# Performance work log

Measured on AMD Instinct MI355X. Metric: run time of the kernel, lower is better.

## Reference

```python
import jax, jax.numpy as jnp
import numpy as np

BLOCK_SIZE = 16
NVFP4_LEVELS = np.array([0.0, 0.5, 1.0, 1.5, 2.0, 3.0, 4.0, 6.0], dtype=np.float32)


def quantize_to_nvfp4(x, block_size=BLOCK_SIZE):
    """NVFP4 fake-quant: per-16-element block, scale = amax/6, round |x| to nearest level."""
    levels = jnp.asarray(NVFP4_LEVELS, dtype=x.dtype)
    orig_shape = x.shape
    xf = x.reshape(-1, block_size)                                   # [nblk, 16]
    amax = jnp.clip(jnp.max(jnp.abs(xf), axis=-1, keepdims=True), 1e-12)
    scale = amax / 6.0                                               # [nblk, 1]
    x_norm = jnp.abs(xf) / scale                                     # in [0, 6]
    idx = jnp.argmin(jnp.abs(x_norm[..., None] - levels), axis=-1)   # nearest level (first on ties, like torch)
    x_q = jnp.sign(xf) * levels[idx] * scale
    return x_q.reshape(orig_shape)


def _magnitude_mask_2_4(w):
    # keep 2 largest-|.| of every group of 4 along in_features (row-wise 2:4)
    out_f, in_f = w.shape
    a = jnp.abs(w).reshape(out_f, in_f // 4, 4)
    thr = jnp.sort(a, axis=-1)[..., 2:3]          # 2nd-largest magnitude in group
    mask = (a >= thr).reshape(out_f, in_f)
    return mask.astype(w.dtype)


def setup_inputs() -> dict:
    key = jax.random.key(0)
    k_x, k_w, k_s, k_a, k_b, k_bias = jax.random.split(key, 6)
    B, S, IN_F, OUT_F, RANK = 2, 2048, 4096, 4096, 32
    x = jax.random.normal(k_x, (B, S, IN_F), dtype=jnp.float32)
    smooth_scale = jax.random.uniform(k_s, (IN_F,), dtype=jnp.float32, minval=0.5, maxval=2.0)
    # realistic calibrated weight: 2:4 magnitude-sparse then NVFP4 fake-quantized
    w = jax.random.normal(k_w, (OUT_F, IN_F), dtype=jnp.float32) * 0.02
    w_sparse = w * _magnitude_mask_2_4(w)
    w_quantized = quantize_to_nvfp4(w_sparse)
    lora_a = jax.random.normal(k_a, (RANK, IN_F), dtype=jnp.float32) * 0.02
    lora_b = jax.random.normal(k_b, (OUT_F, RANK), dtype=jnp.float32) * 0.02
    bias = jax.random.normal(k_bias, (OUT_F,), dtype=jnp.float32)
    return {"x": x, "smooth_scale": smooth_scale, "w_quantized": w_quantized,
            "lora_a": lora_a, "lora_b": lora_b, "bias": bias}


def reference(x, smooth_scale, w_quantized, lora_a, lora_b, bias):
    # x: [B, S, IN], smooth_scale: [IN], w_quantized: [OUT, IN]
    x_smoothed = x * smooth_scale                                    # SmoothQuant activation scaling
    x_q = quantize_to_nvfp4(x_smoothed, BLOCK_SIZE)                  # block fake-quant of activations
    base_out = jnp.einsum('bsi,oi->bso', x_q, w_quantized)           # 2:4-sparse quantized matmul
    svd_out = jnp.einsum('bsr,or->bso',
                         jnp.einsum('bsi,ri->bsr', x_smoothed, lora_a), lora_b)  # low-rank correction
    return base_out + svd_out + bias
```

## Files before the change

### kernel.cpp

```cpp
#include <hip/hip_runtime.h>
#include <hip/hip_bf16.h>
#include <stdint.h>

typedef __attribute__((ext_vector_type(8)))  __bf16 bf16x8;
typedef __attribute__((ext_vector_type(4)))  float  f32x4;

#define KP 4224

__device__ inline void async_copy16(const void* g, void* l) {
  __builtin_amdgcn_global_load_lds((const __attribute__((address_space(1))) void*)g,
                                   (__attribute__((address_space(3))) void*)l, 16, 0, 0);
}

__global__ __launch_bounds__(256) void fused_quant_lora_kernel(
    const float* __restrict__ x, const float* __restrict__ ss,
    const float* __restrict__ la, __bf16* __restrict__ Ab,
    float* __restrict__ Tp) {
  __shared__ float red[4][16][32];
  int tid  = threadIdx.x;
  int m0   = blockIdx.x << 4;
  int by   = blockIdx.y;

  {
    int row = m0 + (tid >> 4);
    int cb0 = tid & 15;
#pragma unroll
    for (int i = 0; i < 2; i++) {
      int col = (by << 9) + ((cb0 + (i << 4)) << 4);
      const float4* xp = (const float4*)(x + ((size_t)row << 12) + col);
      const float4* sp = (const float4*)(ss + col);
      float xs[16];
#pragma unroll
      for (int j = 0; j < 4; j++) {
        float4 xv = xp[j]; float4 sv = sp[j];
        xs[4*j+0] = xv.x * sv.x; xs[4*j+1] = xv.y * sv.y;
        xs[4*j+2] = xv.z * sv.z; xs[4*j+3] = xv.w * sv.w;
      }
      float amax = 0.f;
#pragma unroll
      for (int j = 0; j < 16; j++) amax = fmaxf(amax, fabsf(xs[j]));
      amax = fmaxf(amax, 1e-12f);
      float scale = amax / 6.0f;
      bf16x8 o0, o1;
#pragma unroll
      for (int j = 0; j < 16; j++) {
        float a  = fabsf(xs[j]);
        float xn = a / scale;
        float lvl;
        if (xn < 2.25f) {
          lvl = 0.5f * __builtin_ceilf(__builtin_fmaf(2.0f, xn, -0.5f));
        } else {
          lvl = (xn <= 2.5f) ? 2.0f : (xn <= 3.5f) ? 3.0f
              : (xn <= 5.0f) ? 4.0f : 6.0f;
        }
        float mag = lvl * scale;
        float q = (xs[j] > 0.f) ? mag : ((xs[j] < 0.f) ? -mag : 0.f);
        if (j < 8) o0[j] = (__bf16)q; else o1[j-8] = (__bf16)q;
      }
      __bf16* dst = Ab + (size_t)row * KP + col;
      *(bf16x8*)dst = o0;
      *(bf16x8*)(dst + 8) = o1;
    }
  }

  {
    int wave = tid >> 6, lane = tid & 63;
    int lrow = lane & 15, kg = lane >> 4;
    int kbase = (by << 9) + (wave << 7);
    f32x4 acc0 = {0.f,0.f,0.f,0.f}, acc1 = {0.f,0.f,0.f,0.f};
    const float* xrow = x + ((size_t)(m0 + lrow) << 12);
    const float* a0   = la + ((size_t)lrow << 12);
    const float* a1   = a0 + (16 << 12);
#pragma unroll
    for (int k0 = 0; k0 < 128; k0 += 32) {
      int kk = kbase + k0 + (kg << 3);
      float xv[8], sv[8], v0[8], v1[8];
      *(float4*)&xv[0] = *(const float4*)(xrow + kk);
      *(float4*)&xv[4] = *(const float4*)(xrow + kk + 4);
      *(float4*)&sv[0] = *(const float4*)(ss + kk);
      *(float4*)&sv[4] = *(const float4*)(ss + kk + 4);
      *(float4*)&v0[0] = *(const float4*)(a0 + kk);
      *(float4*)&v0[4] = *(const float4*)(a0 + kk + 4);
      *(float4*)&v1[0] = *(const float4*)(a1 + kk);
      *(float4*)&v1[4] = *(const float4*)(a1 + kk + 4);
      bf16x8 af, b0, b1;
#pragma unroll
      for (int j = 0; j < 8; j++) {
        af[j] = (__bf16)(xv[j] * sv[j]);
        b0[j] = (__bf16)v0[j];
        b1[j] = (__bf16)v1[j];
      }
      acc0 = __builtin_amdgcn_mfma_f32_16x16x32_bf16(af, b0, acc0, 0, 0, 0);
      acc1 = __builtin_amdgcn_mfma_f32_16x16x32_bf16(af, b1, acc1, 0, 0, 0);
    }
#pragma unroll
    for (int r = 0; r < 4; r++) {
      red[wave][kg*4 + r][lrow]      = acc0[r];
      red[wave][kg*4 + r][16 + lrow] = acc1[r];
    }
    __syncthreads();
    for (int o = tid; o < 512; o += 256) {
      int rr = o >> 5, cc = o & 31;
      float s = red[0][rr][cc] + red[1][rr][cc] + red[2][rr][cc] + red[3][rr][cc];
      Tp[((size_t)by * 4096 + m0 + rr) * 32 + cc] = s;
    }
  }
}

__global__ __launch_bounds__(256) void wconv_fix_kernel(const float* __restrict__ w,
                                                        const float* __restrict__ lb,
                                                        const float* __restrict__ Tp,
                                                        __bf16* __restrict__ Bb,
                                                        __bf16* __restrict__ Ab) {
  int b = blockIdx.x;
  if (b < 8448) {
    int id  = b * 256 + threadIdx.x;
    int row = id / 528;
    int g   = id - row * 528;
    bf16x8 v;
    if (g < 512) {
      const float4* wp = (const float4*)(w + ((size_t)row << 12) + (g << 3));
      float4 a = wp[0], bb = wp[1];
      v[0]=(__bf16)a.x;  v[1]=(__bf16)a.y;  v[2]=(__bf16)a.z;  v[3]=(__bf16)a.w;
      v[4]=(__bf16)bb.x; v[5]=(__bf16)bb.y; v[6]=(__bf16)bb.z; v[7]=(__bf16)bb.w;
    } else if (g < 516) {
      const float* p = lb + (size_t)row * 32 + ((g - 512) << 3);
#pragma unroll
      for (int j = 0; j < 8; j++) v[j] = (__bf16)p[j];
    } else {
#pragma unroll
      for (int j = 0; j < 8; j++) v[j] = (__bf16)0.f;
    }
    *(bf16x8*)(Bb + (size_t)row * KP + ((size_t)g << 3)) = v;
  } else {
    int id  = (b - 8448) * 256 + threadIdx.x;
    int row = id >> 5, cc = id & 31;
    float s = 0.f;
#pragma unroll
    for (int kc = 0; kc < 8; kc++)
      s += Tp[((size_t)kc * 4096 + row) * 32 + cc];
    __bf16* dst = Ab + (size_t)row * KP + 4096;
    dst[cc]      = (__bf16)s;
    dst[32 + cc] = (__bf16)0.f;
    dst[64 + cc] = (__bf16)0.f;
    dst[96 + cc] = (__bf16)0.f;
  }
}

#define GBAR() __builtin_amdgcn_s_barrier()
#define PRI1() __builtin_amdgcn_s_setprio(1)
#define PRI0() __builtin_amdgcn_s_setprio(0)
#define WVM(n) asm volatile("s_waitcnt vmcnt(" #n ")" ::: "memory")

#define STG(srcb, dstb, bb, h, t) do {                                         \
    const __bf16* _s = (srcb) + (size_t)(h) * (128 * (size_t)KP)               \
                              + ((size_t)(t) << 6);                            \
    char* _d = (dstb) + ((bb) << 15) + ((h) << 14);                            \
    async_copy16(_s, _d);                                                      \
    async_copy16(_s + 32, _d + 1024);                                          \
  } while (0)

#define LD8(dst, p, off) do { _Pragma("unroll")                                \
  for (int u = 0; u < 8; u++)                                                  \
    dst[u] = *(const bf16x8*)((p) + (((off) + u) << 10)); } while (0)

#define LD4(dst, p, off) do { _Pragma("unroll")                                \
  for (int u = 0; u < 4; u++)                                                  \
    dst[u] = *(const bf16x8*)((p) + (((off) + u) << 10)); } while (0)

#define MMQ(Ar, Br, MFB, NFB) do {                                             \
  _Pragma("unroll") for (int mf = 0; mf < 4; mf++)                             \
  _Pragma("unroll") for (int nf = 0; nf < 2; nf++)                             \
  _Pragma("unroll") for (int ks = 0; ks < 2; ks++)                             \
    acc[(MFB)+mf][(NFB)+nf] = __builtin_amdgcn_mfma_f32_16x16x32_bf16(         \
        Ar[mf*2+ks], Br[nf*2+ks], acc[(MFB)+mf][(NFB)+nf], 0, 0, 0);           \
  } while (0)

__global__ __launch_bounds__(512, 2) void gemm_kernel(const __bf16* __restrict__ A,
                                                      const __bf16* __restrict__ B,
                                                      const float* __restrict__ bias,
                                                      float* __restrict__ C) {
  extern __shared__ char lds[];
  const int tid  = threadIdx.x;
  const int w    = tid >> 6, lane = tid & 63;
  const int ln15 = lane & 15, kg = lane >> 4;
  const int wm   = w >> 2, wn = w & 3;
  const int bid  = blockIdx.x;
  const int sbid = ((bid & 7) << 5) | (bid >> 3);
  const int bm   = sbid >> 4, bn = sbid & 15;
  const size_t m0 = (size_t)bm << 8, n0 = (size_t)bn << 8;

  const int rr = (w << 4) + (lane >> 2);
  const int kk = ((lane & 3) ^ (((lane >> 5) & 1) << 1)) << 3;
  const __bf16* aS = A + (m0 + rr) * (size_t)KP + kk;
  const __bf16* bS = B + (n0 + rr) * (size_t)KP + kk;
  char* dA = lds + (w << 11);
  char* dB = lds + 65536 + (w << 11);

  int inner = (ln15 << 6) + (kg << 4);
  inner ^= (ln15 & 8) << 2;
  const char* pA0 = lds + (wm << 14) + inner;
  const char* pA1 = pA0 + 32768;
  const char* pB0 = lds + 65536 + (wn << 13) + inner;
  const char* pB1 = pB0 + 32768;

  bf16x8 Ax[8], Ay[8], Bg0[4], Bg1[4];
  f32x4 acc[8][4];
#pragma unroll
  for (int i = 0; i < 8; i++)
#pragma unroll
    for (int j = 0; j < 4; j++) acc[i][j] = (f32x4){0.f, 0.f, 0.f, 0.f};

  STG(bS, dB, 0, 0, 0); STG(bS, dB, 0, 1, 0);
  STG(aS, dA, 0, 0, 0); STG(aS, dA, 0, 1, 0);
  STG(bS, dB, 1, 0, 1); STG(bS, dB, 1, 1, 1);
  WVM(4);
  GBAR();
  LD8(Ax, pA0, 0); LD4(Bg0, pB0, 0);

#pragma unroll 1
  for (int i = 0; i < 32; i++) {
    const int t1 = 2*i + 1, t2 = 2*i + 2, t3 = 2*i + 3;
    GBAR();
    STG(aS, dA, 1, 0, t1);
    LD8(Ay, pA0, 8); LD4(Bg1, pB0, 4);
    PRI1(); MMQ(Ax, Bg0, 0, 0); PRI0();
    GBAR();
    STG(aS, dA, 1, 1, t1);
    PRI1(); MMQ(Ax, Bg1, 0, 2); PRI0();
    GBAR();
    STG(bS, dB, 0, 0, t2);
    PRI1(); MMQ(Ay, Bg0, 4, 0); PRI0();
    WVM(2);
    GBAR();
    STG(bS, dB, 0, 1, t2);
    LD8(Ax, pA1, 0); LD4(Bg0, pB1, 0);
    PRI1(); MMQ(Ay, Bg1, 4, 2); PRI0();
    GBAR();
    STG(aS, dA, 0, 0, t2);
    LD8(Ay, pA1, 8); LD4(Bg1, pB1, 4);
    PRI1(); MMQ(Ax, Bg0, 0, 0); PRI0();
    GBAR();
    STG(aS, dA, 0, 1, t2);
    PRI1(); MMQ(Ax, Bg1, 0, 2); PRI0();
    GBAR();
    STG(bS, dB, 1, 0, t3);
    PRI1(); MMQ(Ay, Bg0, 4, 0); PRI0();
    WVM(2);
    GBAR();
    STG(bS, dB, 1, 1, t3);
    LD8(Ax, pA0, 0); LD4(Bg0, pB0, 0);
    PRI1(); MMQ(Ay, Bg1, 4, 2); PRI0();
  }

  GBAR();
  STG(aS, dA, 1, 0, 65);
  LD8(Ay, pA0, 8); LD4(Bg1, pB0, 4);
  PRI1(); MMQ(Ax, Bg0, 0, 0); PRI0();
  GBAR();
  STG(aS, dA, 1, 1, 65);
  PRI1(); MMQ(Ax, Bg1, 0, 2); PRI0();
  GBAR();
  PRI1(); MMQ(Ay, Bg0, 4, 0); PRI0();
  WVM(0);
  GBAR();
  LD8(Ax, pA1, 0); LD4(Bg0, pB1, 0);
  PRI1(); MMQ(Ay, Bg1, 4, 2); PRI0();
  GBAR();
  LD8(Ay, pA1, 8); LD4(Bg1, pB1, 4);
  PRI1(); MMQ(Ax, Bg0, 0, 0); PRI0();
  GBAR();
  PRI1(); MMQ(Ax, Bg1, 0, 2); PRI0();
  GBAR();
  PRI1(); MMQ(Ay, Bg0, 4, 0); PRI0();
  GBAR();
  PRI1(); MMQ(Ay, Bg1, 4, 2); PRI0();

  const int    colb = (int)n0 + (wn << 6) + ln15;
  const size_t rowb = m0 + ((size_t)wm << 7) + (kg << 2);
#pragma unroll
  for (int nf = 0; nf < 4; nf++) {
    const int col = colb + (nf << 4);
    const float bv = bias[col];
#pragma unroll
    for (int mf = 0; mf < 8; mf++) {
      const size_t r0 = rowb + ((size_t)mf << 4);
#pragma unroll
      for (int q = 0; q < 4; q++)
        C[(r0 + q) * 4096 + col] = acc[mf][nf][q] + bv;
    }
  }
}

extern "C" void kernel_launch(void* const* d_in, const int* in_sizes, int n_in,
                              void* d_out, int out_size, void* d_ws, size_t ws_size,
                              hipStream_t stream) {
  const float* x    = (const float*)d_in[0];
  const float* ss   = (const float*)d_in[1];
  const float* w    = (const float*)d_in[2];
  const float* la   = (const float*)d_in[3];
  const float* lb   = (const float*)d_in[4];
  const float* bias = (const float*)d_in[5];
  float* out = (float*)d_out;

  __bf16* Ab = (__bf16*)d_ws;
  __bf16* Bb = Ab + (size_t)4096 * KP;
  float* Tp = out;

  static bool s_attr = false;
  if (!s_attr) {
    hipFuncSetAttribute((const void*)gemm_kernel,
                        hipFuncAttributeMaxDynamicSharedMemorySize, 131072);
    s_attr = true;
  }

  fused_quant_lora_kernel<<<dim3(256, 8), 256, 0, stream>>>(x, ss, la, Ab, Tp);
  wconv_fix_kernel<<<8960, 256, 0, stream>>>(w, lb, Tp, Bb, Ab);
  gemm_kernel<<<256, 512, 131072, stream>>>(Ab, Bb, bias, out);
}
```

Baseline: 310.1 us.

## Merge prep kernels and compute full-K LoRA projection per block

```diff
diff --git a/kernel.cpp b/kernel.cpp
--- a/kernel.cpp
+++ b/kernel.cpp
@@ -12,16 +12,18 @@
                                    (__attribute__((address_space(3))) void*)l, 16, 0, 0);
 }
 
-__global__ __launch_bounds__(256) void fused_quant_lora_kernel(
+__global__ __launch_bounds__(256) void prep_kernel(
     const float* __restrict__ x, const float* __restrict__ ss,
-    const float* __restrict__ la, __bf16* __restrict__ Ab,
-    float* __restrict__ Tp) {
+    const float* __restrict__ w, const float* __restrict__ la,
+    const float* __restrict__ lb, __bf16* __restrict__ Ab,
+    __bf16* __restrict__ Bb) {
   __shared__ float red[4][16][32];
-  int tid  = threadIdx.x;
-  int m0   = blockIdx.x << 4;
-  int by   = blockIdx.y;
-
-  {
+  int b   = blockIdx.x;
+  int tid = threadIdx.x;
+
+  if (b < 2048) {
+    int m0 = (b >> 3) << 4;
+    int by = b & 7;
     int row = m0 + (tid >> 4);
     int cb0 = tid & 15;
 #pragma unroll
@@ -61,19 +63,36 @@
       *(bf16x8*)dst = o0;
       *(bf16x8*)(dst + 8) = o1;
     }
-  }
-
-  {
+  } else if (b < 10496) {
+    int id  = (b - 2048) * 256 + tid;
+    int row = id / 528;
+    int g   = id - row * 528;
+    bf16x8 v;
+    if (g < 512) {
+      const float4* wp = (const float4*)(w + ((size_t)row << 12) + (g << 3));
+      float4 a = wp[0], bb = wp[1];
+      v[0]=(__bf16)a.x;  v[1]=(__bf16)a.y;  v[2]=(__bf16)a.z;  v[3]=(__bf16)a.w;
+      v[4]=(__bf16)bb.x; v[5]=(__bf16)bb.y; v[6]=(__bf16)bb.z; v[7]=(__bf16)bb.w;
+    } else if (g < 516) {
+      const float* p = lb + (size_t)row * 32 + ((g - 512) << 3);
+#pragma unroll
+      for (int j = 0; j < 8; j++) v[j] = (__bf16)p[j];
+    } else {
+#pragma unroll
+      for (int j = 0; j < 8; j++) v[j] = (__bf16)0.f;
+    }
+    *(bf16x8*)(Bb + (size_t)row * KP + ((size_t)g << 3)) = v;
+  } else {
+    int j16  = (b - 10496) << 4;
     int wave = tid >> 6, lane = tid & 63;
     int lrow = lane & 15, kg = lane >> 4;
-    int kbase = (by << 9) + (wave << 7);
     f32x4 acc0 = {0.f,0.f,0.f,0.f}, acc1 = {0.f,0.f,0.f,0.f};
-    const float* xrow = x + ((size_t)(m0 + lrow) << 12);
+    const float* xrow = x + ((size_t)(j16 + lrow) << 12);
     const float* a0   = la + ((size_t)lrow << 12);
     const float* a1   = a0 + (16 << 12);
-#pragma unroll
-    for (int k0 = 0; k0 < 128; k0 += 32) {
-      int kk = kbase + k0 + (kg << 3);
+#pragma unroll 4
+    for (int k0 = 0; k0 < 32; k0++) {
+      int kk = (wave << 10) + (k0 << 5) + (kg << 3);
       float xv[8], sv[8], v0[8], v1[8];
       *(float4*)&xv[0] = *(const float4*)(xrow + kk);
       *(float4*)&xv[4] = *(const float4*)(xrow + kk + 4);
@@ -85,10 +104,10 @@
       *(float4*)&v1[4] = *(const float4*)(a1 + kk + 4);
       bf16x8 af, b0, b1;
 #pragma unroll
-      for (int j = 0; j < 8; j++) {
-        af[j] = (__bf16)(xv[j] * sv[j]);
-        b0[j] = (__bf16)v0[j];
-        b1[j] = (__bf16)v1[j];
+      for (int q = 0; q < 8; q++) {
+        af[q] = (__bf16)(xv[q] * sv[q]);
+        b0[q] = (__bf16)v0[q];
+        b1[q] = (__bf16)v1[q];
       }
       acc0 = __builtin_amdgcn_mfma_f32_16x16x32_bf16(af, b0, acc0, 0, 0, 0);
       acc1 = __builtin_amdgcn_mfma_f32_16x16x32_bf16(af, b1, acc1, 0, 0, 0);
@@ -102,48 +121,12 @@
     for (int o = tid; o < 512; o += 256) {
       int rr = o >> 5, cc = o & 31;
       float s = red[0][rr][cc] + red[1][rr][cc] + red[2][rr][cc] + red[3][rr][cc];
-      Tp[((size_t)by * 4096 + m0 + rr) * 32 + cc] = s;
-    }
-  }
-}
-
-__global__ __launch_bounds__(256) void wconv_fix_kernel(const float* __restrict__ w,
-                                                        const float* __restrict__ lb,
-                                                        const float* __restrict__ Tp,
-                                                        __bf16* __restrict__ Bb,
-                                                        __bf16* __restrict__ Ab) {
-  int b = blockIdx.x;
-  if (b < 8448) {
-    int id  = b * 256 + threadIdx.x;
-    int row = id / 528;
-    int g   = id - row * 528;
-    bf16x8 v;
-    if (g < 512) {
-      const float4* wp = (const float4*)(w + ((size_t)row << 12) + (g << 3));
-      float4 a = wp[0], bb = wp[1];
-      v[0]=(__bf16)a.x;  v[1]=(__bf16)a.y;  v[2]=(__bf16)a.z;  v[3]=(__bf16)a.w;
-      v[4]=(__bf16)bb.x; v[5]=(__bf16)bb.y; v[6]=(__bf16)bb.z; v[7]=(__bf16)bb.w;
-    } else if (g < 516) {
-      const float* p = lb + (size_t)row * 32 + ((g - 512) << 3);
-#pragma unroll
-      for (int j = 0; j < 8; j++) v[j] = (__bf16)p[j];
-    } else {
-#pragma unroll
-      for (int j = 0; j < 8; j++) v[j] = (__bf16)0.f;
-    }
-    *(bf16x8*)(Bb + (size_t)row * KP + ((size_t)g << 3)) = v;
-  } else {
-    int id  = (b - 8448) * 256 + threadIdx.x;
-    int row = id >> 5, cc = id & 31;
-    float s = 0.f;
-#pragma unroll
-    for (int kc = 0; kc < 8; kc++)
-      s += Tp[((size_t)kc * 4096 + row) * 32 + cc];
-    __bf16* dst = Ab + (size_t)row * KP + 4096;
-    dst[cc]      = (__bf16)s;
-    dst[32 + cc] = (__bf16)0.f;
-    dst[64 + cc] = (__bf16)0.f;
-    dst[96 + cc] = (__bf16)0.f;
+      __bf16* dst = Ab + (size_t)(j16 + rr) * KP + 4096;
+      dst[cc]      = (__bf16)s;
+      dst[32 + cc] = (__bf16)0.f;
+      dst[64 + cc] = (__bf16)0.f;
+      dst[96 + cc] = (__bf16)0.f;
+    }
   }
 }
 
@@ -305,7 +288,6 @@
 
   __bf16* Ab = (__bf16*)d_ws;
   __bf16* Bb = Ab + (size_t)4096 * KP;
-  float* Tp = out;
 
   static bool s_attr = false;
   if (!s_attr) {
@@ -314,7 +296,6 @@
     s_attr = true;
   }
 
-  fused_quant_lora_kernel<<<dim3(256, 8), 256, 0, stream>>>(x, ss, la, Ab, Tp);
-  wconv_fix_kernel<<<8960, 256, 0, stream>>>(w, lb, Tp, Bb, Ab);
+  prep_kernel<<<10752, 256, 0, stream>>>(x, ss, w, la, lb, Ab, Bb);
   gemm_kernel<<<256, 512, 131072, stream>>>(Ab, Bb, bias, out);
 }
```

After: 368.6 us. 18.9% more time.
